# Optimization experiments

Hardware: AMD Instinct MI355X
Metric: run time of the kernel (lower is better)

## Reference

```python
import jax, jax.numpy as jnp
import numpy as np

V, D, T, H, L, B = 50257, 1024, 1024, 16, 6, 2
HS = D // H  # 64
EPS = 1e-5


def setup_inputs() -> dict:
    key = jax.random.key(0)
    ks = jax.random.split(key, 16)
    s = 0.02
    n = lambda k, sh: jax.random.normal(k, sh, jnp.float32) * s
    return {
        'idx': jax.random.randint(ks[0], (B, T), 0, V),
        'targets': jax.random.randint(ks[1], (B, T), 0, V),
        'tok_emb': n(ks[2], (V, D)),
        'pos_emb': n(ks[3], (T, D)),
        'wq': n(ks[4], (L, H, D, HS)),
        'wk': n(ks[5], (L, H, D, HS)),
        'wv': n(ks[6], (L, H, D, HS)),
        'wproj': n(ks[7], (L, D, D)),
        'bproj': jnp.zeros((L, D), jnp.float32),
        'ln1_g': jnp.ones((L, D), jnp.float32),
        'ln1_b': jnp.zeros((L, D), jnp.float32),
        'ln2_g': jnp.ones((L, D), jnp.float32),
        'ln2_b': jnp.zeros((L, D), jnp.float32),
        'w1': n(ks[8], (L, D, 4 * D)),
        'b1': jnp.zeros((L, 4 * D), jnp.float32),
        'w2': n(ks[9], (L, 4 * D, D)),
        'b2': jnp.zeros((L, D), jnp.float32),
        'lnf_g': jnp.ones((D,), jnp.float32),
        'lnf_b': jnp.zeros((D,), jnp.float32),
        'lm_w': n(ks[10], (D, V)),
        'lm_b': jnp.zeros((V,), jnp.float32),
    }


def _layernorm(x, g, b):
    mu = jnp.mean(x, axis=-1, keepdims=True)
    var = jnp.var(x, axis=-1, keepdims=True)
    return (x - mu) * jax.lax.rsqrt(var + EPS) * g + b


def _forward(idx, targets, tok_emb, pos_emb, wq, wk, wv, wproj, bproj,
             ln1_g, ln1_b, ln2_g, ln2_b, w1, b1, w2, b2, lnf_g, lnf_b, lm_w, lm_b):
    t = idx.shape[1]
    x = tok_emb[idx] + pos_emb[:t]  # [B,T,D]
    causal = jnp.tril(jnp.ones((t, t), bool))  # [T,T]
    neg_inf = jnp.float32(-jnp.inf)

    def block(x, p):
        (wq_l, wk_l, wv_l, wp_l, bp_l, g1, b1_ln, g2, b2_ln, wf1, bf1, wf2, bf2) = p
        h = _layernorm(x, g1, b1_ln)
        q = jnp.einsum('btd,hdk->bhtk', h, wq_l)
        k = jnp.einsum('btd,hdk->bhtk', h, wk_l)
        v = jnp.einsum('btd,hdk->bhtk', h, wv_l)
        scores = jnp.einsum('bhtk,bhsk->bhts', q, k) * (HS ** -0.5)
        scores = jnp.where(causal, scores, neg_inf)
        attn = jax.nn.softmax(scores, axis=-1)  # dropout p=0.0
        o = jnp.einsum('bhts,bhsk->bhtk', attn, v)
        o = o.transpose(0, 2, 1, 3).reshape(x.shape[0], t, H * HS)  # concat heads
        x = x + o @ wp_l + bp_l
        h2 = _layernorm(x, g2, b2_ln)
        x = x + jax.nn.relu(h2 @ wf1 + bf1) @ wf2 + bf2
        return x, None

    x, _ = jax.lax.scan(block, x, (wq, wk, wv, wproj, bproj,
                                   ln1_g, ln1_b, ln2_g, ln2_b, w1, b1, w2, b2))
    x = _layernorm(x, lnf_g, lnf_b)
    logits = x @ lm_w + lm_b  # [B,T,V]
    logp = jax.nn.log_softmax(logits, axis=-1)
    loss = -jnp.mean(jnp.take_along_axis(logp, targets[..., None], axis=-1))
    return logits, loss


def reference(idx, targets, tok_emb, pos_emb, wq, wk, wv, wproj, bproj,
              ln1_g, ln1_b, ln2_g, ln2_b, w1, b1, w2, b2, lnf_g, lnf_b, lm_w, lm_b):
    return _forward(idx, targets, tok_emb, pos_emb, wq, wk, wv, wproj, bproj,
                    ln1_g, ln1_b, ln2_g, ln2_b, w1, b1, w2, b2, lnf_g, lnf_b, lm_w, lm_b)
```

## Files before the change

kernel.cpp:

```cpp
#include <hip/hip_runtime.h>
#include <cstdint>
#include <cstddef>

typedef unsigned short u16;
typedef unsigned int u32;
typedef __bf16 bf16x8 __attribute__((ext_vector_type(8)));
typedef float f32x4 __attribute__((ext_vector_type(4)));
typedef short short8_t __attribute__((ext_vector_type(8)));

#define NV 50257
#define NVPAD 50304
#define NBLK_LM 393
#define ND 1024
#define NT 1024
#define NH 16
#define NL 6
#define NB 2
#define NM 2048
#define NF 4096
#define EPSLN 1e-5f

__device__ __forceinline__ u16 f2bf(float f) {
    unsigned u = __float_as_uint(f);
    return (u16)((u + 0x7fffu + ((u >> 16) & 1u)) >> 16);
}
__device__ __forceinline__ float bf2f(u16 h) {
    return __uint_as_float(((unsigned)h) << 16);
}
__device__ __forceinline__ u32 pack2bf(float lo, float hi) {
    return (u32)f2bf(lo) | ((u32)f2bf(hi) << 16);
}

__device__ __forceinline__ void gload_lds16(const u16* g, u16* l) {
    __builtin_amdgcn_global_load_lds((const __attribute__((address_space(1))) void*)g,
                                     (__attribute__((address_space(3))) void*)l, 16, 0, 0);
}

__device__ __forceinline__ float wave_reduce_sum(float v) {
#pragma unroll
    for (int off = 32; off >= 1; off >>= 1) v += __shfl_xor(v, off, 64);
    return v;
}

__global__ __launch_bounds__(256) void k_embed(const int* __restrict__ idx,
                                               const float* __restrict__ tok,
                                               const float* __restrict__ pos,
                                               float* __restrict__ x) {
    int m = blockIdx.x;
    int t = m & (NT - 1);
    int tokid = idx[m];
    int d = threadIdx.x * 4;
    float4 a = *(const float4*)(tok + (size_t)tokid * ND + d);
    float4 p = *(const float4*)(pos + (size_t)t * ND + d);
    a.x += p.x; a.y += p.y; a.z += p.z; a.w += p.w;
    *(float4*)(x + (size_t)m * ND + d) = a;
}

__global__ __launch_bounds__(256) void k_layernorm(const float* __restrict__ x,
                                                   const float* __restrict__ g,
                                                   const float* __restrict__ b,
                                                   u16* __restrict__ outb) {
    int m = blockIdx.x;
    int d = threadIdx.x * 4;
    const float4 v = *(const float4*)(x + (size_t)m * ND + d);
    float s = v.x + v.y + v.z + v.w;
    float q = v.x * v.x + v.y * v.y + v.z * v.z + v.w * v.w;
    s = wave_reduce_sum(s);
    q = wave_reduce_sum(q);
    __shared__ float ss[4], sq[4];
    int lane = threadIdx.x & 63, w = threadIdx.x >> 6;
    if (lane == 0) { ss[w] = s; sq[w] = q; }
    __syncthreads();
    s = ss[0] + ss[1] + ss[2] + ss[3];
    q = sq[0] + sq[1] + sq[2] + sq[3];
    float mu = s * (1.0f / ND);
    float var = q * (1.0f / ND) - mu * mu;
    float rstd = rsqrtf(var + EPSLN);
    float4 gg = *(const float4*)(g + d);
    float4 bb = *(const float4*)(b + d);
    ushort4 pk;
    pk.x = f2bf((v.x - mu) * rstd * gg.x + bb.x);
    pk.y = f2bf((v.y - mu) * rstd * gg.y + bb.y);
    pk.z = f2bf((v.z - mu) * rstd * gg.z + bb.z);
    pk.w = f2bf((v.w - mu) * rstd * gg.w + bb.w);
    *(ushort4*)(outb + (size_t)m * ND + d) = pk;
}

__global__ __launch_bounds__(256) void k_wtrans(const float* __restrict__ W,
                                                u16* __restrict__ Wt,
                                                int K, int N, int Npad, int hs, int ld) {
    __shared__ float t[32][33];
    const int nb = blockIdx.x << 5, kb = blockIdx.y << 5;
    const int tx = threadIdx.x & 31, tq = threadIdx.x >> 5;
    const int n = nb + tx;
    if (n < N) {
        const int head = n / hs, nc = n - head * hs;
        const float* src = W + (size_t)head * K * hs + nc;
#pragma unroll
        for (int i = 0; i < 4; ++i)
            t[(tq << 2) + i][tx] = src[(size_t)(kb + (tq << 2) + i) * ld];
    } else {
#pragma unroll
        for (int i = 0; i < 4; ++i) t[(tq << 2) + i][tx] = 0.f;
    }
    __syncthreads();
#pragma unroll
    for (int i = 0; i < 4; ++i) {
        const int nn = nb + (tq << 2) + i;
        if (nn < Npad) Wt[(size_t)nn * K + kb + tx] = f2bf(t[tx][(tq << 2) + i]);
    }
}

__global__ __launch_bounds__(256) void k_wtrans_qkv(const float* __restrict__ Wq,
                                                    const float* __restrict__ Wk,
                                                    const float* __restrict__ Wv,
                                                    u16* __restrict__ Wt) {
    __shared__ float t[32][33];
    const float* W = (blockIdx.z == 0) ? Wq : (blockIdx.z == 1) ? Wk : Wv;
    u16* dst = Wt + (size_t)blockIdx.z * ND * ND;
    const int nb = blockIdx.x << 5, kb = blockIdx.y << 5;
    const int tx = threadIdx.x & 31, tq = threadIdx.x >> 5;
    const int n = nb + tx;
    {
        const int head = n >> 6, nc = n & 63;
        const float* src = W + (size_t)head * ND * 64 + nc;
#pragma unroll
        for (int i = 0; i < 4; ++i)
            t[(tq << 2) + i][tx] = src[(size_t)(kb + (tq << 2) + i) * 64];
    }
    __syncthreads();
#pragma unroll
    for (int i = 0; i < 4; ++i) {
        const int nn = nb + (tq << 2) + i;
        dst[(size_t)nn * ND + kb + tx] = f2bf(t[tx][(tq << 2) + i]);
    }
}

__global__ __launch_bounds__(256) void k_vtrans(const u16* __restrict__ qkv,
                                                u16* __restrict__ vt) {
    __shared__ u16 L[64][72];
    const int tt = blockIdx.x, bh = blockIdx.y;
    const int b = bh >> 4, h = bh & 15;
    const int tid = threadIdx.x;
    const int tr = tid >> 2, dc = (tid & 3) << 4;
    const u16* src = qkv + (size_t)(b * NT + tt * 64 + tr) * 3072 + 2048 + h * 64 + dc;
    short8_t v0 = *(const short8_t*)src;
    short8_t v1 = *(const short8_t*)(src + 8);
#pragma unroll
    for (int j = 0; j < 8; ++j) { L[tr][dc + j] = (u16)v0[j]; L[tr][dc + 8 + j] = (u16)v1[j]; }
    __syncthreads();
    const int dr = tid >> 2, tc = (tid & 3) << 4;
    union { u16 us[16]; short8_t v[2]; } tmp;
#pragma unroll
    for (int j = 0; j < 16; ++j) tmp.us[j] = L[tc + j][dr];
    u16* dst = vt + ((size_t)bh * 64 + dr) * NT + tt * 64 + tc;
    *(short8_t*)dst = tmp.v[0];
    *(short8_t*)(dst + 8) = tmp.v[1];
}

__global__ __launch_bounds__(512) void k_gemm_lm(
    const u16* __restrict__ A, const u16* __restrict__ Bt,
    const float* __restrict__ bias,
    float* __restrict__ Cf,
    float* __restrict__ pmax_g, float* __restrict__ psum_g,
    int K, int N, int ldc)
{
    __shared__ u16 As[2][256 * 32];
    __shared__ u16 Bs[2][128 * 32];
    const int lin = blockIdx.y * 8 + blockIdx.x;
    const int nwg = (int)gridDim.y * 8;
    const int cpx = nwg >> 3;
    const int swz = (lin & 7) * cpx + (lin >> 3);
    const int m0 = (swz & 7) * 256;
    const int n0 = (swz >> 3) * 128;
    const int tid = threadIdx.x;
    const int lane = tid & 63, w = tid >> 6;
    const int wr = w >> 1, wc = w & 1;
    const int lr = lane & 15, kg = lane >> 4;

    const int srow = lane >> 2;
    const int scol = (((lane & 3) ^ ((lane >> 3) & 3)) << 3);
    const u16* gA0 = A + (size_t)(m0 + w * 16 + srow) * K + scol;
    const u16* gA1 = gA0 + (size_t)128 * K;
    const u16* gB0 = Bt + (size_t)(n0 + w * 16 + srow) * K + scol;

    f32x4 acc[4][4] = {};
    const int nt = K >> 5;

    gload_lds16(gA0, &As[0][w * 512]);
    gload_lds16(gA1, &As[0][4096 + w * 512]);
    gload_lds16(gB0, &Bs[0][w * 512]);
    __syncthreads();

    int cur = 0;
    for (int t = 0; t < nt; ++t) {
        if (t + 1 < nt) {
            const int ko = (t + 1) << 5;
            gload_lds16(gA0 + ko, &As[cur ^ 1][w * 512]);
            gload_lds16(gA1 + ko, &As[cur ^ 1][4096 + w * 512]);
            gload_lds16(gB0 + ko, &Bs[cur ^ 1][w * 512]);
        }
        bf16x8 af[4], bfr[4];
        const int rsw = ((kg ^ ((lr >> 1) & 3)) << 3);
#pragma unroll
        for (int mi = 0; mi < 4; ++mi)
            af[mi] = *(const bf16x8*)&As[cur][(wr * 64 + mi * 16 + lr) * 32 + rsw];
#pragma unroll
        for (int ni = 0; ni < 4; ++ni)
            bfr[ni] = *(const bf16x8*)&Bs[cur][(wc * 64 + ni * 16 + lr) * 32 + rsw];
#pragma unroll
        for (int mi = 0; mi < 4; ++mi)
#pragma unroll
            for (int ni = 0; ni < 4; ++ni)
                acc[mi][ni] = __builtin_amdgcn_mfma_f32_16x16x32_bf16(af[mi], bfr[ni], acc[mi][ni], 0, 0, 0);
        __syncthreads();
        cur ^= 1;
    }

#pragma unroll
    for (int mi = 0; mi < 4; ++mi)
#pragma unroll
        for (int ni = 0; ni < 4; ++ni)
#pragma unroll
            for (int r = 0; r < 4; ++r) {
                const int row = m0 + wr * 64 + mi * 16 + kg * 4 + r;
                const int col = n0 + wc * 64 + ni * 16 + lr;
                if (col >= N) continue;
                acc[mi][ni][r] += bias[col];
                Cf[(size_t)row * ldc + col] = acc[mi][ni][r];
            }

    float* redm = (float*)As;
    float* reds = redm + 512;
#pragma unroll
    for (int mi = 0; mi < 4; ++mi)
#pragma unroll
        for (int r = 0; r < 4; ++r) {
            float vmax = -3.0e38f;
#pragma unroll
            for (int ni = 0; ni < 4; ++ni) {
                const int col = n0 + wc * 64 + ni * 16 + lr;
                vmax = fmaxf(vmax, (col < N) ? acc[mi][ni][r] : -3.0e38f);
            }
            vmax = fmaxf(vmax, __shfl_xor(vmax, 1));
            vmax = fmaxf(vmax, __shfl_xor(vmax, 2));
            vmax = fmaxf(vmax, __shfl_xor(vmax, 4));
            vmax = fmaxf(vmax, __shfl_xor(vmax, 8));
            if (lr == 0) redm[wc * 256 + wr * 64 + mi * 16 + kg * 4 + r] = vmax;
        }
    __syncthreads();
#pragma unroll
    for (int mi = 0; mi < 4; ++mi)
#pragma unroll
        for (int r = 0; r < 4; ++r) {
            const int rloc = wr * 64 + mi * 16 + kg * 4 + r;
            const float M = fmaxf(redm[rloc], redm[256 + rloc]);
            float s = 0.f;
#pragma unroll
            for (int ni = 0; ni < 4; ++ni) {
                const int col = n0 + wc * 64 + ni * 16 + lr;
                if (col < N) s += __expf(acc[mi][ni][r] - M);
            }
            s += __shfl_xor(s, 1);
            s += __shfl_xor(s, 2);
            s += __shfl_xor(s, 4);
            s += __shfl_xor(s, 8);
            if (lr == 0) reds[wc * 256 + rloc] = s;
        }
    __syncthreads();
    if (tid < 256) {
        const float M = fmaxf(redm[tid], redm[256 + tid]);
        const float S = reds[tid] + reds[256 + tid];
        const int nblk = n0 >> 7;
        pmax_g[(size_t)nblk * NM + m0 + tid] = M;
        psum_g[(size_t)nblk * NM + m0 + tid] = S;
    }
}

template <bool RELU, bool NBOUND, bool OUTBF16>
__global__ __launch_bounds__(256) void k_mfma_gemm(
    const u16* __restrict__ A, const u16* __restrict__ Bt,
    const float* __restrict__ bias,
    float* __restrict__ Cf, u16* __restrict__ Cb,
    int K, int N, int ldc)
{
    __shared__ u16 As[2][128 * 32];
    __shared__ u16 Bs[2][128 * 32];
    const int lin = blockIdx.y * 16 + blockIdx.x;
    const int nwg = (int)gridDim.y * 16;
    const int cpx = nwg >> 3;
    const int swz = (lin & 7) * cpx + (lin >> 3);
    const int m0 = (swz & 15) * 128;
    const int n0 = (swz >> 4) * 128;
    const int tid = threadIdx.x;
    const int lane = tid & 63, wv = tid >> 6;
    const int wr = wv >> 1, wc = wv & 1;
    const int lr = lane & 15, kg = lane >> 4;

    const int srow = lane >> 2;
    const int scol = (((lane & 3) ^ ((lane >> 3) & 3)) << 3);
    const u16* gA0 = A + (size_t)(m0 + wv * 16 + srow) * K + scol;
    const u16* gA1 = gA0 + (size_t)64 * K;
    const u16* gB0 = Bt + (size_t)(n0 + wv * 16 + srow) * K + scol;
    const u16* gB1 = gB0 + (size_t)64 * K;

    f32x4 acc[4][4] = {};
    const int nt = K >> 5;

    gload_lds16(gA0, &As[0][wv * 512]);
    gload_lds16(gA1, &As[0][2048 + wv * 512]);
    gload_lds16(gB0, &Bs[0][wv * 512]);
    gload_lds16(gB1, &Bs[0][2048 + wv * 512]);
    __syncthreads();

    int cur = 0;
    for (int t = 0; t < nt; ++t) {
        if (t + 1 < nt) {
            const int ko = (t + 1) << 5;
            gload_lds16(gA0 + ko, &As[cur ^ 1][wv * 512]);
            gload_lds16(gA1 + ko, &As[cur ^ 1][2048 + wv * 512]);
            gload_lds16(gB0 + ko, &Bs[cur ^ 1][wv * 512]);
            gload_lds16(gB1 + ko, &Bs[cur ^ 1][2048 + wv * 512]);
        }
        bf16x8 af[4], bfr[4];
        const int rsw = ((kg ^ ((lr >> 1) & 3)) << 3);
#pragma unroll
        for (int mi = 0; mi < 4; ++mi) {
            const int R = wr * 64 + mi * 16 + lr;
            af[mi] = *(const bf16x8*)&As[cur][R * 32 + rsw];
        }
#pragma unroll
        for (int ni = 0; ni < 4; ++ni) {
            const int R = wc * 64 + ni * 16 + lr;
            bfr[ni] = *(const bf16x8*)&Bs[cur][R * 32 + rsw];
        }
#pragma unroll
        for (int mi = 0; mi < 4; ++mi)
#pragma unroll
            for (int ni = 0; ni < 4; ++ni)
                acc[mi][ni] = __builtin_amdgcn_mfma_f32_16x16x32_bf16(af[mi], bfr[ni], acc[mi][ni], 0, 0, 0);
        __syncthreads();
        cur ^= 1;
    }
#pragma unroll
    for (int mi = 0; mi < 4; ++mi) {
#pragma unroll
        for (int ni = 0; ni < 4; ++ni) {
#pragma unroll
            for (int r = 0; r < 4; ++r) {
                const int row = m0 + wr * 64 + mi * 16 + kg * 4 + r;
                const int col = n0 + wc * 64 + ni * 16 + lr;
                if (NBOUND && col >= N) continue;
                float c = acc[mi][ni][r];
                if (bias) c += bias[col];
                if (RELU) c = fmaxf(c, 0.f);
                if (OUTBF16) Cb[(size_t)row * ldc + col] = f2bf(c);
                else         Cf[(size_t)row * ldc + col] = c;
            }
        }
    }
}

__global__ __launch_bounds__(256) void k_gemm_ksplit(
    const u16* __restrict__ A, const u16* __restrict__ Bt,
    float* __restrict__ P,
    int Khalf, int Ktot, int ldc)
{
    __shared__ u16 As[2][128 * 32];
    __shared__ u16 Bs[2][128 * 32];
    const int z = blockIdx.z;
    const int lin = blockIdx.y * 16 + blockIdx.x;
    const int nwg = (int)gridDim.y * 16;
    const int cpx = nwg >> 3;
    const int swz = (lin & 7) * cpx + (lin >> 3);
    const int m0 = (swz & 15) * 128;
    const int n0 = (swz >> 4) * 128;
    const int tid = threadIdx.x;
    const int lane = tid & 63, wv = tid >> 6;
    const int wr = wv >> 1, wc = wv & 1;
    const int lr = lane & 15, kg = lane >> 4;

    const int srow = lane >> 2;
    const int scol = (((lane & 3) ^ ((lane >> 3) & 3)) << 3);
    const int koff = z * Khalf;
    const u16* gA0 = A + (size_t)(m0 + wv * 16 + srow) * Ktot + koff + scol;
    const u16* gA1 = gA0 + (size_t)64 * Ktot;
    const u16* gB0 = Bt + (size_t)(n0 + wv * 16 + srow) * Ktot + koff + scol;
    const u16* gB1 = gB0 + (size_t)64 * Ktot;
    float* Pz = P + (size_t)z * NM * ldc;

    f32x4 acc[4][4] = {};
    const int nt = Khalf >> 5;

    gload_lds16(gA0, &As[0][wv * 512]);
    gload_lds16(gA1, &As[0][2048 + wv * 512]);
    gload_lds16(gB0, &Bs[0][wv * 512]);
    gload_lds16(gB1, &Bs[0][2048 + wv * 512]);
    __syncthreads();

    int cur = 0;
    for (int t = 0; t < nt; ++t) {
        if (t + 1 < nt) {
            const int ko = (t + 1) << 5;
            gload_lds16(gA0 + ko, &As[cur ^ 1][wv * 512]);
            gload_lds16(gA1 + ko, &As[cur ^ 1][2048 + wv * 512]);
            gload_lds16(gB0 + ko, &Bs[cur ^ 1][wv * 512]);
            gload_lds16(gB1 + ko, &Bs[cur ^ 1][2048 + wv * 512]);
        }
        bf16x8 af[4], bfr[4];
        const int rsw = ((kg ^ ((lr >> 1) & 3)) << 3);
#pragma unroll
        for (int mi = 0; mi < 4; ++mi) {
            const int R = wr * 64 + mi * 16 + lr;
            af[mi] = *(const bf16x8*)&As[cur][R * 32 + rsw];
        }
#pragma unroll
        for (int ni = 0; ni < 4; ++ni) {
            const int R = wc * 64 + ni * 16 + lr;
            bfr[ni] = *(const bf16x8*)&Bs[cur][R * 32 + rsw];
        }
#pragma unroll
        for (int mi = 0; mi < 4; ++mi)
#pragma unroll
            for (int ni = 0; ni < 4; ++ni)
                acc[mi][ni] = __builtin_amdgcn_mfma_f32_16x16x32_bf16(af[mi], bfr[ni], acc[mi][ni], 0, 0, 0);
        __syncthreads();
        cur ^= 1;
    }
#pragma unroll
    for (int mi = 0; mi < 4; ++mi)
#pragma unroll
        for (int ni = 0; ni < 4; ++ni)
#pragma unroll
            for (int r = 0; r < 4; ++r) {
                const int row = m0 + wr * 64 + mi * 16 + kg * 4 + r;
                const int col = n0 + wc * 64 + ni * 16 + lr;
                Pz[(size_t)row * ldc + col] = acc[mi][ni][r];
            }
}

__global__ __launch_bounds__(256) void k_combine(const float* __restrict__ p,
                                                 const float* __restrict__ bias,
                                                 float* __restrict__ x) {
    const int m = blockIdx.x;
    const int d = threadIdx.x * 4;
    float4 a  = *(const float4*)(x + (size_t)m * ND + d);
    float4 q0 = *(const float4*)(p + (size_t)m * ND + d);
    float4 q1 = *(const float4*)(p + (size_t)NM * ND + (size_t)m * ND + d);
    float4 bb = *(const float4*)(bias + d);
    a.x += q0.x + q1.x + bb.x;
    a.y += q0.y + q1.y + bb.y;
    a.z += q0.z + q1.z + bb.z;
    a.w += q0.w + q1.w + bb.w;
    *(float4*)(x + (size_t)m * ND + d) = a;
}

template <bool RELU, bool RESID, bool OUTBF16>
__global__ __launch_bounds__(256) void k_gemm_n64(
    const u16* __restrict__ A, const u16* __restrict__ Bt,
    const float* __restrict__ bias, const float* __restrict__ resid,
    float* __restrict__ Cf, u16* __restrict__ Cb,
    int K, int ldc)
{
    __shared__ u16 As[2][128 * 32];
    __shared__ u16 Bs[2][64 * 32];
    const int lin = blockIdx.y * 16 + blockIdx.x;
    const int nwg = (int)gridDim.y * 16;
    const int cpx = nwg >> 3;
    const int swz = (lin & 7) * cpx + (lin >> 3);
    const int m0 = (swz & 15) * 128;
    const int n0 = (swz >> 4) * 64;
    const int tid = threadIdx.x;
    const int lane = tid & 63, wv = tid >> 6;
    const int lr = lane & 15, kg = lane >> 4;

    const int srow = lane >> 2;
    const int scol = (((lane & 3) ^ ((lane >> 3) & 3)) << 3);
    const u16* gA0 = A + (size_t)(m0 + wv * 32 + srow) * K + scol;
    const u16* gA1 = gA0 + (size_t)16 * K;
    const u16* gB0 = Bt + (size_t)(n0 + wv * 16 + srow) * K + scol;

    f32x4 acc[2][4] = {};
    const int nt = K >> 5;

    gload_lds16(gA0, &As[0][wv * 1024]);
    gload_lds16(gA1, &As[0][wv * 1024 + 512]);
    gload_lds16(gB0, &Bs[0][wv * 512]);
    __syncthreads();

    int cur = 0;
    for (int t = 0; t < nt; ++t) {
        if (t + 1 < nt) {
            const int ko = (t + 1) << 5;
            gload_lds16(gA0 + ko, &As[cur ^ 1][wv * 1024]);
            gload_lds16(gA1 + ko, &As[cur ^ 1][wv * 1024 + 512]);
            gload_lds16(gB0 + ko, &Bs[cur ^ 1][wv * 512]);
        }
        bf16x8 af[2], bfr[4];
        const int rsw = ((kg ^ ((lr >> 1) & 3)) << 3);
#pragma unroll
        for (int mi = 0; mi < 2; ++mi)
            af[mi] = *(const bf16x8*)&As[cur][(wv * 32 + mi * 16 + lr) * 32 + rsw];
#pragma unroll
        for (int ni = 0; ni < 4; ++ni)
            bfr[ni] = *(const bf16x8*)&Bs[cur][(ni * 16 + lr) * 32 + rsw];
#pragma unroll
        for (int mi = 0; mi < 2; ++mi)
#pragma unroll
            for (int ni = 0; ni < 4; ++ni)
                acc[mi][ni] = __builtin_amdgcn_mfma_f32_16x16x32_bf16(af[mi], bfr[ni], acc[mi][ni], 0, 0, 0);
        __syncthreads();
        cur ^= 1;
    }
#pragma unroll
    for (int mi = 0; mi < 2; ++mi) {
#pragma unroll
        for (int ni = 0; ni < 4; ++ni) {
#pragma unroll
            for (int r = 0; r < 4; ++r) {
                const int row = m0 + wv * 32 + mi * 16 + kg * 4 + r;
                const int col = n0 + ni * 16 + lr;
                float c = acc[mi][ni][r];
                if (bias) c += bias[col];
                if (RELU) c = fmaxf(c, 0.f);
                if (RESID) c += resid[(size_t)row * ldc + col];
                if (OUTBF16) Cb[(size_t)row * ldc + col] = f2bf(c);
                else         Cf[(size_t)row * ldc + col] = c;
            }
        }
    }
}

__global__ __launch_bounds__(256) void k_attn_mfma(const u16* __restrict__ qkv,
                                                   const u16* __restrict__ vt,
                                                   u16* __restrict__ ob) {
    const int qt = (blockIdx.y < 16) ? (int)blockIdx.x : 15 - (int)blockIdx.x;
    const int bh = blockIdx.y;
    const int b = bh >> 4, h = bh & 15;
    const int tid = threadIdx.x;
    const int lane = tid & 63, w = tid >> 6;
    const int lr = lane & 15, kg = lane >> 4;

    __shared__ u16 Qs[64 * 64];
    __shared__ u16 Ks[2][64 * 64];
    __shared__ u16 Vs[2][64 * 64];

    const int srow8 = lane >> 3;
    const int csw = ((lane & 7) ^ srow8) << 3;

    {
        const int r0 = w * 8 + srow8;
        gload_lds16(qkv + (size_t)(b * NT + qt * 64 + r0) * 3072 + h * 64 + csw, &Qs[w * 512]);
        gload_lds16(qkv + (size_t)(b * NT + qt * 64 + 32 + r0) * 3072 + h * 64 + csw, &Qs[2048 + w * 512]);
    }
#define STAGE_KV(bb, st)                                                                            \
    {                                                                                               \
        const int r0_ = w * 8 + srow8;                                                              \
        gload_lds16(qkv + (size_t)(b * NT + (st) * 64 + r0_) * 3072 + 1024 + h * 64 + csw,          \
                    &Ks[bb][w * 512]);                                                              \
        gload_lds16(qkv + (size_t)(b * NT + (st) * 64 + 32 + r0_) * 3072 + 1024 + h * 64 + csw,     \
                    &Ks[bb][2048 + w * 512]);                                                       \
        gload_lds16(vt + ((size_t)bh * 64 + r0_) * NT + (st) * 64 + csw, &Vs[bb][w * 512]);         \
        gload_lds16(vt + ((size_t)bh * 64 + 32 + r0_) * NT + (st) * 64 + csw,                       \
                    &Vs[bb][2048 + w * 512]);                                                       \
    }
    STAGE_KV(0, 0);
    __syncthreads();

    bf16x8 qf[2];
    {
        const int qrow = w * 16 + lr;
#pragma unroll
        for (int ds_ = 0; ds_ < 2; ++ds_)
            qf[ds_] = *(const bf16x8*)&Qs[qrow * 64 + ((((ds_ << 2) + kg) ^ (lr & 7)) << 3)];
    }

    float mstate = -3.0e38f, lstate = 0.f;
    f32x4 acc_o[4] = {};
    const int qg = qt * 64 + w * 16 + lr;

    int cur = 0;
    for (int st = 0; st <= qt; ++st) {
        if (st < qt) STAGE_KV(cur ^ 1, st + 1);
        const bool diag = (st == qt);
        const int milim = diag ? w : 3;

        f32x4 acc_s[4] = {};
#pragma unroll
        for (int mi = 0; mi < 4; ++mi) {
            if (mi <= milim) {
                const int srw = mi * 16 + lr;
#pragma unroll
                for (int ds_ = 0; ds_ < 2; ++ds_) {
                    bf16x8 kf = *(const bf16x8*)&Ks[cur][srw * 64 + ((((ds_ << 2) + kg) ^ (lr & 7)) << 3)];
                    acc_s[mi] = __builtin_amdgcn_mfma_f32_16x16x32_bf16(kf, qf[ds_], acc_s[mi], 0, 0, 0);
                }
            }
        }
        float tilemax = -3.0e38f;
#pragma unroll
        for (int mi = 0; mi < 4; ++mi)
#pragma unroll
            for (int r = 0; r < 4; ++r) {
                float x_ = acc_s[mi][r] * 0.125f;
                const int sg = st * 64 + mi * 16 + kg * 4 + r;
                if (mi > milim || sg > qg) x_ = -3.0e38f;
                acc_s[mi][r] = x_;
                tilemax = fmaxf(tilemax, x_);
            }
        tilemax = fmaxf(tilemax, __shfl_xor(tilemax, 16));
        tilemax = fmaxf(tilemax, __shfl_xor(tilemax, 32));
        const float mnew = fmaxf(mstate, tilemax);
        const float rfac = __expf(mstate - mnew);
        mstate = mnew;

        float psum = 0.f;
        u32 pk[4][2];
#pragma unroll
        for (int mi = 0; mi < 4; ++mi) {
            float p0 = __expf(acc_s[mi][0] - mnew);
            float p1 = __expf(acc_s[mi][1] - mnew);
            float p2 = __expf(acc_s[mi][2] - mnew);
            float p3 = __expf(acc_s[mi][3] - mnew);
            psum += p0 + p1 + p2 + p3;
            pk[mi][0] = pack2bf(p0, p1);
            pk[mi][1] = pack2bf(p2, p3);
        }
        psum += __shfl_xor(psum, 16);
        psum += __shfl_xor(psum, 32);
        lstate = lstate * rfac + psum;

        float rf[4];
#pragma unroll
        for (int r = 0; r < 4; ++r) rf[r] = __shfl(rfac, kg * 4 + r);
#pragma unroll
        for (int ni = 0; ni < 4; ++ni)
#pragma unroll
            for (int r = 0; r < 4; ++r) acc_o[ni][r] *= rf[r];

        const int src0 = ((kg & 1) << 5) + lr;
        const int src1 = src0 + 16;
#pragma unroll
        for (int ks_ = 0; ks_ < 2; ++ks_) {
            const u32 lo_a = __shfl((int)pk[ks_ * 2][0], src0);
            const u32 lo_b = __shfl((int)pk[ks_ * 2][1], src0);
            const u32 lo_c = __shfl((int)pk[ks_ * 2][0], src1);
            const u32 lo_d = __shfl((int)pk[ks_ * 2][1], src1);
            const u32 hi_a = __shfl((int)pk[ks_ * 2 + 1][0], src0);
            const u32 hi_b = __shfl((int)pk[ks_ * 2 + 1][1], src0);
            const u32 hi_c = __shfl((int)pk[ks_ * 2 + 1][0], src1);
            const u32 hi_d = __shfl((int)pk[ks_ * 2 + 1][1], src1);
            union { u32 u[4]; bf16x8 v; } pa;
            pa.u[0] = (kg & 2) ? hi_a : lo_a;
            pa.u[1] = (kg & 2) ? hi_b : lo_b;
            pa.u[2] = (kg & 2) ? hi_c : lo_c;
            pa.u[3] = (kg & 2) ? hi_d : lo_d;
#pragma unroll
            for (int ni = 0; ni < 4; ++ni) {
                const int drow = ni * 16 + lr;
                bf16x8 vf = *(const bf16x8*)&Vs[cur][drow * 64 + ((((ks_ << 2) + kg) ^ (lr & 7)) << 3)];
                acc_o[ni] = __builtin_amdgcn_mfma_f32_16x16x32_bf16(pa.v, vf, acc_o[ni], 0, 0, 0);
            }
        }
        __syncthreads();
        cur ^= 1;
    }

    float il[4];
#pragma unroll
    for (int r = 0; r < 4; ++r) il[r] = 1.0f / __shfl(lstate, kg * 4 + r);
#pragma unroll
    for (int ni = 0; ni < 4; ++ni)
#pragma unroll
        for (int r = 0; r < 4; ++r) {
            const int q2 = qt * 64 + w * 16 + kg * 4 + r;
            ob[(size_t)(b * NT + q2) * ND + h * 64 + ni * 16 + lr] = f2bf(acc_o[ni][r] * il[r]);
        }
#undef STAGE_KV
}

__global__ __launch_bounds__(256) void k_losscombine(const float* __restrict__ pmax,
                                                     const float* __restrict__ psum,
                                                     const float* __restrict__ logits,
                                                     const int* __restrict__ targets,
                                                     float* __restrict__ rl) {
    const int row = blockIdx.x * 4 + (threadIdx.x >> 6);
    const int lane = threadIdx.x & 63;
    float M = -3.0e38f;
    for (int j = lane; j < NBLK_LM; j += 64) M = fmaxf(M, pmax[(size_t)j * NM + row]);
#pragma unroll
    for (int off = 32; off >= 1; off >>= 1) M = fmaxf(M, __shfl_xor(M, off, 64));
    float S = 0.f;
    for (int j = lane; j < NBLK_LM; j += 64)
        S += psum[(size_t)j * NM + row] * __expf(pmax[(size_t)j * NM + row] - M);
    S = wave_reduce_sum(S);
    if (lane == 0)
        rl[row] = M + logf(S) - logits[(size_t)row * NV + targets[row]];
}

__global__ __launch_bounds__(256) void k_lossreduce(const float* __restrict__ rl,
                                                    float* __restrict__ out_loss) {
    int tid = threadIdx.x;
    float s = 0.f;
    for (int j = tid; j < NM; j += 256) s += rl[j];
    s = wave_reduce_sum(s);
    __shared__ float sv[4];
    int lane = tid & 63, w = tid >> 6;
    if (lane == 0) sv[w] = s;
    __syncthreads();
    if (tid == 0) out_loss[0] = (sv[0] + sv[1] + sv[2] + sv[3]) * (1.0f / NM);
}

extern "C" void kernel_launch(void* const* d_in, const int* in_sizes, int n_in,
                              void* d_out, int out_size, void* d_ws, size_t ws_size,
                              hipStream_t stream) {
    const int* idx      = (const int*)d_in[0];
    const int* targets  = (const int*)d_in[1];
    const float* tok    = (const float*)d_in[2];
    const float* pos    = (const float*)d_in[3];
    const float* wq     = (const float*)d_in[4];
    const float* wk     = (const float*)d_in[5];
    const float* wv     = (const float*)d_in[6];
    const float* wproj  = (const float*)d_in[7];
    const float* bproj  = (const float*)d_in[8];
    const float* ln1_g  = (const float*)d_in[9];
    const float* ln1_b  = (const float*)d_in[10];
    const float* ln2_g  = (const float*)d_in[11];
    const float* ln2_b  = (const float*)d_in[12];
    const float* w1     = (const float*)d_in[13];
    const float* b1     = (const float*)d_in[14];
    const float* w2     = (const float*)d_in[15];
    const float* b2     = (const float*)d_in[16];
    const float* lnf_g  = (const float*)d_in[17];
    const float* lnf_b  = (const float*)d_in[18];
    const float* lm_w   = (const float*)d_in[19];
    const float* lm_b   = (const float*)d_in[20];
    float* out = (float*)d_out;

    char* wsb = (char*)d_ws;
    auto alloc = [&](size_t bytes) { char* p = wsb; wsb += (bytes + 255) & ~(size_t)255; return p; };
    float* x     = (float*)alloc((size_t)NM * ND * 4);
    u16* h_bf    = (u16*)  alloc((size_t)NM * ND * 2);
    float* rl    = (float*)alloc((size_t)NM * 4);
    float* pmax  = (float*)alloc((size_t)NBLK_LM * NM * 4);
    float* psum  = (float*)alloc((size_t)NBLK_LM * NM * 4);
    char* region = (char*)alloc((size_t)NVPAD * ND * 2);
    u16* qkv_bf = (u16*)(region);
    u16* vt_bf  = (u16*)(region + ((size_t)12 << 20));
    u16* ob_bf  = (u16*)(region + ((size_t)16 << 20));
    u16* hid_bf = (u16*)(region + ((size_t)20 << 20));
    u16* wqkv_t = (u16*)(region + ((size_t)36 << 20));
    u16* wp_t   = (u16*)(region + ((size_t)42 << 20));
    u16* w1_t   = (u16*)(region + ((size_t)44 << 20));
    u16* w2_t   = (u16*)(region + ((size_t)52 << 20));
    float* p01  = (float*)(region + ((size_t)60 << 20));
    u16* lm_t   = (u16*)(region);

    k_embed<<<NM, 256, 0, stream>>>(idx, tok, pos, x);

    for (int l = 0; l < NL; ++l) {
        const float* wq_l = wq + (size_t)l * NH * ND * 64;
        const float* wk_l = wk + (size_t)l * NH * ND * 64;
        const float* wv_l = wv + (size_t)l * NH * ND * 64;
        const float* wp_l = wproj + (size_t)l * ND * ND;
        const float* bp_l = bproj + (size_t)l * ND;
        const float* w1_l = w1 + (size_t)l * ND * NF;
        const float* b1_l = b1 + (size_t)l * NF;
        const float* w2_l = w2 + (size_t)l * NF * ND;
        const float* b2_l = b2 + (size_t)l * ND;

        k_layernorm<<<NM, 256, 0, stream>>>(x, ln1_g + (size_t)l * ND, ln1_b + (size_t)l * ND, h_bf);

        k_wtrans_qkv<<<dim3(32, 32, 3), 256, 0, stream>>>(wq_l, wk_l, wv_l, wqkv_t);
        k_mfma_gemm<false, false, true><<<dim3(16, 24), 256, 0, stream>>>(
            h_bf, wqkv_t, nullptr, nullptr, qkv_bf, ND, 3 * ND, 3 * ND);

        k_vtrans<<<dim3(NT / 64, NB * NH), 256, 0, stream>>>(qkv_bf, vt_bf);
        k_attn_mfma<<<dim3(NT / 64, NB * NH), 256, 0, stream>>>(qkv_bf, vt_bf, ob_bf);

        k_wtrans<<<dim3(ND / 32, ND / 32), 256, 0, stream>>>(wp_l, wp_t, ND, ND, ND, ND, ND);
        k_gemm_n64<false, true, false><<<dim3(16, 16), 256, 0, stream>>>(
            ob_bf, wp_t, bp_l, x, x, nullptr, ND, ND);

        k_layernorm<<<NM, 256, 0, stream>>>(x, ln2_g + (size_t)l * ND, ln2_b + (size_t)l * ND, h_bf);

        k_wtrans<<<dim3(NF / 32, ND / 32), 256, 0, stream>>>(w1_l, w1_t, ND, NF, NF, NF, NF);
        k_mfma_gemm<true, false, true><<<dim3(16, 32), 256, 0, stream>>>(
            h_bf, w1_t, b1_l, nullptr, hid_bf, ND, NF, NF);

        k_wtrans<<<dim3(ND / 32, NF / 32), 256, 0, stream>>>(w2_l, w2_t, NF, ND, ND, ND, ND);
        k_gemm_ksplit<<<dim3(16, 8, 2), 256, 0, stream>>>(
            hid_bf, w2_t, p01, NF / 2, NF, ND);
        k_combine<<<NM, 256, 0, stream>>>(p01, b2_l, x);
    }

    k_layernorm<<<NM, 256, 0, stream>>>(x, lnf_g, lnf_b, h_bf);

    k_wtrans<<<dim3(NVPAD / 32, ND / 32), 256, 0, stream>>>(lm_w, lm_t, ND, NV, NVPAD, NV, NV);
    k_gemm_lm<<<dim3(8, NVPAD / 128), 512, 0, stream>>>(
        h_bf, lm_t, lm_b, out, pmax, psum, ND, NV, NV);

    k_losscombine<<<NM / 4, 256, 0, stream>>>(pmax, psum, out, targets, rl);
    k_lossreduce<<<1, 256, 0, stream>>>(rl, out + (size_t)NM * NV);
}
```

Before: 1.663 ms.

## Generalize LM-head GEMM to 256x128 tiles for FFN, merge weight transposes

Turns the 512-thread 256x128-tile LM-head GEMM into a template with optional ReLU, bf16 output, K-split and softmax-partial epilogues. It then runs the FFN up-projection with it, and the down-projection as a 4-way K-split with a four-input combine kernel. The three per-layer weight transposes (proj, w1, w2) are merged into one launch, cutting launch count. Bigger tiles give more data reuse per block but fewer blocks (256 for the FFN1 GEMM), and the 4-way split adds extra fp32 partial traffic.

After: 1.613 ms. -3.0%, faster.

```diff
diff --git a/kernel.cpp b/kernel.cpp
--- a/kernel.cpp
+++ b/kernel.cpp
@@ -136,6 +136,31 @@
     }
 }
 
+__global__ __launch_bounds__(256) void k_wtrans3(const float* __restrict__ Wp,
+                                                 const float* __restrict__ W1,
+                                                 const float* __restrict__ W2,
+                                                 u16* __restrict__ Wpt,
+                                                 u16* __restrict__ W1t,
+                                                 u16* __restrict__ W2t) {
+    __shared__ float t[32][33];
+    int bid = blockIdx.x;
+    const float* W; u16* Wt; int K, N, nb, kb;
+    if (bid < 1024)      { W = Wp; Wt = Wpt; K = ND; N = ND; bid -= 0;
+                           nb = (bid & 31) << 5; kb = (bid >> 5) << 5; }
+    else if (bid < 5120) { W = W1; Wt = W1t; K = ND; N = NF; bid -= 1024;
+                           nb = (bid & 127) << 5; kb = (bid >> 7) << 5; }
+    else                 { W = W2; Wt = W2t; K = NF; N = ND; bid -= 5120;
+                           nb = (bid & 31) << 5; kb = (bid >> 5) << 5; }
+    const int tx = threadIdx.x & 31, tq = threadIdx.x >> 5;
+#pragma unroll
+    for (int i = 0; i < 4; ++i)
+        t[(tq << 2) + i][tx] = W[(size_t)(kb + (tq << 2) + i) * N + nb + tx];
+    __syncthreads();
+#pragma unroll
+    for (int i = 0; i < 4; ++i)
+        Wt[(size_t)(nb + (tq << 2) + i) * K + kb + tx] = f2bf(t[tx][(tq << 2) + i]);
+}
+
 __global__ __launch_bounds__(256) void k_vtrans(const u16* __restrict__ qkv,
                                                 u16* __restrict__ vt) {
     __shared__ u16 L[64][72];
@@ -158,17 +183,18 @@
     *(short8_t*)(dst + 8) = tmp.v[1];
 }
 
-__global__ __launch_bounds__(512) void k_gemm_lm(
+template <bool RELU, bool NBOUND, bool PART, bool KSPLIT, bool OUTBF16>
+__global__ __launch_bounds__(512) void k_gemm_big(
     const u16* __restrict__ A, const u16* __restrict__ Bt,
     const float* __restrict__ bias,
-    float* __restrict__ Cf,
+    float* __restrict__ Cf, u16* __restrict__ Cb,
     float* __restrict__ pmax_g, float* __restrict__ psum_g,
-    int K, int N, int ldc)
+    int Ksub, int Ktot, int N, int ldc)
 {
     __shared__ u16 As[2][256 * 32];
     __shared__ u16 Bs[2][128 * 32];
-    const int lin = blockIdx.y * 8 + blockIdx.x;
-    const int nwg = (int)gridDim.y * 8;
+    const int lin = blockIdx.y * (int)gridDim.x + blockIdx.x;
+    const int nwg = (int)gridDim.x * (int)gridDim.y;
     const int cpx = nwg >> 3;
     const int swz = (lin & 7) * cpx + (lin >> 3);
     const int m0 = (swz & 7) * 256;
@@ -180,12 +206,13 @@
 
     const int srow = lane >> 2;
     const int scol = (((lane & 3) ^ ((lane >> 3) & 3)) << 3);
-    const u16* gA0 = A + (size_t)(m0 + w * 16 + srow) * K + scol;
-    const u16* gA1 = gA0 + (size_t)128 * K;
-    const u16* gB0 = Bt + (size_t)(n0 + w * 16 + srow) * K + scol;
+    const int koff = KSPLIT ? (int)blockIdx.z * Ksub : 0;
+    const u16* gA0 = A + (size_t)(m0 + w * 16 + srow) * Ktot + koff + scol;
+    const u16* gA1 = gA0 + (size_t)128 * Ktot;
+    const u16* gB0 = Bt + (size_t)(n0 + w * 16 + srow) * Ktot + koff + scol;
 
     f32x4 acc[4][4] = {};
-    const int nt = K >> 5;
+    const int nt = Ksub >> 5;
 
     gload_lds16(gA0, &As[0][w * 512]);
     gload_lds16(gA1, &As[0][4096 + w * 512]);
@@ -217,6 +244,7 @@
         cur ^= 1;
     }
 
+    float* Cz = KSPLIT ? (Cf + (size_t)blockIdx.z * NM * ldc) : Cf;
 #pragma unroll
     for (int mi = 0; mi < 4; ++mi)
 #pragma unroll
@@ -225,55 +253,61 @@
             for (int r = 0; r < 4; ++r) {
                 const int row = m0 + wr * 64 + mi * 16 + kg * 4 + r;
                 const int col = n0 + wc * 64 + ni * 16 + lr;
-                if (col >= N) continue;
-                acc[mi][ni][r] += bias[col];
-                Cf[(size_t)row * ldc + col] = acc[mi][ni][r];
+                if (NBOUND && col >= N) continue;
+                float c = acc[mi][ni][r];
+                if (bias) c += bias[col];
+                if (RELU) c = fmaxf(c, 0.f);
+                if (PART) acc[mi][ni][r] = c;
+                if (OUTBF16) Cb[(size_t)row * ldc + col] = f2bf(c);
+                else         Cz[(size_t)row * ldc + col] = c;
             }
 
-    float* redm = (float*)As;
-    float* reds = redm + 512;
-#pragma unroll
-    for (int mi = 0; mi < 4; ++mi)
-#pragma unroll
-        for (int r = 0; r < 4; ++r) {
-            float vmax = -3.0e38f;
-#pragma unroll
-            for (int ni = 0; ni < 4; ++ni) {
-                const int col = n0 + wc * 64 + ni * 16 + lr;
-                vmax = fmaxf(vmax, (col < N) ? acc[mi][ni][r] : -3.0e38f);
+    if constexpr (PART) {
+        float* redm = (float*)As;
+        float* reds = redm + 512;
+#pragma unroll
+        for (int mi = 0; mi < 4; ++mi)
+#pragma unroll
+            for (int r = 0; r < 4; ++r) {
+                float vmax = -3.0e38f;
+#pragma unroll
+                for (int ni = 0; ni < 4; ++ni) {
+                    const int col = n0 + wc * 64 + ni * 16 + lr;
+                    vmax = fmaxf(vmax, (col < N) ? acc[mi][ni][r] : -3.0e38f);
+                }
+                vmax = fmaxf(vmax, __shfl_xor(vmax, 1));
+                vmax = fmaxf(vmax, __shfl_xor(vmax, 2));
+                vmax = fmaxf(vmax, __shfl_xor(vmax, 4));
+                vmax = fmaxf(vmax, __shfl_xor(vmax, 8));
+                if (lr == 0) redm[wc * 256 + wr * 64 + mi * 16 + kg * 4 + r] = vmax;
             }
-            vmax = fmaxf(vmax, __shfl_xor(vmax, 1));
-            vmax = fmaxf(vmax, __shfl_xor(vmax, 2));
-            vmax = fmaxf(vmax, __shfl_xor(vmax, 4));
-            vmax = fmaxf(vmax, __shfl_xor(vmax, 8));
-            if (lr == 0) redm[wc * 256 + wr * 64 + mi * 16 + kg * 4 + r] = vmax;
-        }
-    __syncthreads();
-#pragma unroll
-    for (int mi = 0; mi < 4; ++mi)
-#pragma unroll
-        for (int r = 0; r < 4; ++r) {
-            const int rloc = wr * 64 + mi * 16 + kg * 4 + r;
-            const float M = fmaxf(redm[rloc], redm[256 + rloc]);
-            float s = 0.f;
-#pragma unroll
-            for (int ni = 0; ni < 4; ++ni) {
-                const int col = n0 + wc * 64 + ni * 16 + lr;
-                if (col < N) s += __expf(acc[mi][ni][r] - M);
+        __syncthreads();
+#pragma unroll
+        for (int mi = 0; mi < 4; ++mi)
+#pragma unroll
+            for (int r = 0; r < 4; ++r) {
+                const int rloc = wr * 64 + mi * 16 + kg * 4 + r;
+                const float M = fmaxf(redm[rloc], redm[256 + rloc]);
+                float s = 0.f;
+#pragma unroll
+                for (int ni = 0; ni < 4; ++ni) {
+                    const int col = n0 + wc * 64 + ni * 16 + lr;
+                    if (col < N) s += __expf(acc[mi][ni][r] - M);
+                }
+                s += __shfl_xor(s, 1);
+                s += __shfl_xor(s, 2);
+                s += __shfl_xor(s, 4);
+                s += __shfl_xor(s, 8);
+                if (lr == 0) reds[wc * 256 + rloc] = s;
             }
-            s += __shfl_xor(s, 1);
-            s += __shfl_xor(s, 2);
-            s += __shfl_xor(s, 4);
-            s += __shfl_xor(s, 8);
-            if (lr == 0) reds[wc * 256 + rloc] = s;
-        }
-    __syncthreads();
-    if (tid < 256) {
-        const float M = fmaxf(redm[tid], redm[256 + tid]);
-        const float S = reds[tid] + reds[256 + tid];
-        const int nblk = n0 >> 7;
-        pmax_g[(size_t)nblk * NM + m0 + tid] = M;
-        psum_g[(size_t)nblk * NM + m0 + tid] = S;
+        __syncthreads();
+        if (tid < 256) {
+            const float M = fmaxf(redm[tid], redm[256 + tid]);
+            const float S = reds[tid] + reds[256 + tid];
+            const int nblk = n0 >> 7;
+            pmax_g[(size_t)nblk * NM + m0 + tid] = M;
+            psum_g[(size_t)nblk * NM + m0 + tid] = S;
+        }
     }
 }
 
@@ -361,98 +395,23 @@
     }
 }
 
-__global__ __launch_bounds__(256) void k_gemm_ksplit(
-    const u16* __restrict__ A, const u16* __restrict__ Bt,
-    float* __restrict__ P,
-    int Khalf, int Ktot, int ldc)
-{
-    __shared__ u16 As[2][128 * 32];
-    __shared__ u16 Bs[2][128 * 32];
-    const int z = blockIdx.z;
-    const int lin = blockIdx.y * 16 + blockIdx.x;
-    const int nwg = (int)gridDim.y * 16;
-    const int cpx = nwg >> 3;
-    const int swz = (lin & 7) * cpx + (lin >> 3);
-    const int m0 = (swz & 15) * 128;
-    const int n0 = (swz >> 4) * 128;
-    const int tid = threadIdx.x;
-    const int lane = tid & 63, wv = tid >> 6;
-    const int wr = wv >> 1, wc = wv & 1;
-    const int lr = lane & 15, kg = lane >> 4;
-
-    const int srow = lane >> 2;
-    const int scol = (((lane & 3) ^ ((lane >> 3) & 3)) << 3);
-    const int koff = z * Khalf;
-    const u16* gA0 = A + (size_t)(m0 + wv * 16 + srow) * Ktot + koff + scol;
-    const u16* gA1 = gA0 + (size_t)64 * Ktot;
-    const u16* gB0 = Bt + (size_t)(n0 + wv * 16 + srow) * Ktot + koff + scol;
-    const u16* gB1 = gB0 + (size_t)64 * Ktot;
-    float* Pz = P + (size_t)z * NM * ldc;
-
-    f32x4 acc[4][4] = {};
-    const int nt = Khalf >> 5;
-
-    gload_lds16(gA0, &As[0][wv * 512]);
-    gload_lds16(gA1, &As[0][2048 + wv * 512]);
-    gload_lds16(gB0, &Bs[0][wv * 512]);
-    gload_lds16(gB1, &Bs[0][2048 + wv * 512]);
-    __syncthreads();
-
-    int cur = 0;
-    for (int t = 0; t < nt; ++t) {
-        if (t + 1 < nt) {
-            const int ko = (t + 1) << 5;
-            gload_lds16(gA0 + ko, &As[cur ^ 1][wv * 512]);
-            gload_lds16(gA1 + ko, &As[cur ^ 1][2048 + wv * 512]);
-            gload_lds16(gB0 + ko, &Bs[cur ^ 1][wv * 512]);
-            gload_lds16(gB1 + ko, &Bs[cur ^ 1][2048 + wv * 512]);
-        }
-        bf16x8 af[4], bfr[4];
-        const int rsw = ((kg ^ ((lr >> 1) & 3)) << 3);
-#pragma unroll
-        for (int mi = 0; mi < 4; ++mi) {
-            const int R = wr * 64 + mi * 16 + lr;
-            af[mi] = *(const bf16x8*)&As[cur][R * 32 + rsw];
-        }
-#pragma unroll
-        for (int ni = 0; ni < 4; ++ni) {
-            const int R = wc * 64 + ni * 16 + lr;
-            bfr[ni] = *(const bf16x8*)&Bs[cur][R * 32 + rsw];
-        }
-#pragma unroll
-        for (int mi = 0; mi < 4; ++mi)
-#pragma unroll
-            for (int ni = 0; ni < 4; ++ni)
-                acc[mi][ni] = __builtin_amdgcn_mfma_f32_16x16x32_bf16(af[mi], bfr[ni], acc[mi][ni], 0, 0, 0);
-        __syncthreads();
-        cur ^= 1;
-    }
-#pragma unroll
-    for (int mi = 0; mi < 4; ++mi)
-#pragma unroll
-        for (int ni = 0; ni < 4; ++ni)
-#pragma unroll
-            for (int r = 0; r < 4; ++r) {
-                const int row = m0 + wr * 64 + mi * 16 + kg * 4 + r;
-                const int col = n0 + wc * 64 + ni * 16 + lr;
-                Pz[(size_t)row * ldc + col] = acc[mi][ni][r];
-            }
-}
-
-__global__ __launch_bounds__(256) void k_combine(const float* __restrict__ p,
-                                                 const float* __restrict__ bias,
-                                                 float* __restrict__ x) {
+__global__ __launch_bounds__(256) void k_combine4(const float* __restrict__ p,
+                                                  const float* __restrict__ bias,
+                                                  float* __restrict__ x) {
     const int m = blockIdx.x;
     const int d = threadIdx.x * 4;
-    float4 a  = *(const float4*)(x + (size_t)m * ND + d);
-    float4 q0 = *(const float4*)(p + (size_t)m * ND + d);
-    float4 q1 = *(const float4*)(p + (size_t)NM * ND + (size_t)m * ND + d);
+    const size_t off = (size_t)m * ND + d;
+    float4 a  = *(const float4*)(x + off);
+    float4 q0 = *(const float4*)(p + off);
+    float4 q1 = *(const float4*)(p + (size_t)NM * ND + off);
+    float4 q2 = *(const float4*)(p + (size_t)2 * NM * ND + off);
+    float4 q3 = *(const float4*)(p + (size_t)3 * NM * ND + off);
     float4 bb = *(const float4*)(bias + d);
-    a.x += q0.x + q1.x + bb.x;
-    a.y += q0.y + q1.y + bb.y;
-    a.z += q0.z + q1.z + bb.z;
-    a.w += q0.w + q1.w + bb.w;
-    *(float4*)(x + (size_t)m * ND + d) = a;
+    a.x += ((q0.x + q1.x) + (q2.x + q3.x)) + bb.x;
+    a.y += ((q0.y + q1.y) + (q2.y + q3.y)) + bb.y;
+    a.z += ((q0.z + q1.z) + (q2.z + q3.z)) + bb.z;
+    a.w += ((q0.w + q1.w) + (q2.w + q3.w)) + bb.w;
+    *(float4*)(x + off) = a;
 }
 
 template <bool RELU, bool RESID, bool OUTBF16>
@@ -753,7 +712,7 @@
     u16* wp_t   = (u16*)(region + ((size_t)42 << 20));
     u16* w1_t   = (u16*)(region + ((size_t)44 << 20));
     u16* w2_t   = (u16*)(region + ((size_t)52 << 20));
-    float* p01  = (float*)(region + ((size_t)60 << 20));
+    float* p03  = (float*)(region + ((size_t)60 << 20));
     u16* lm_t   = (u16*)(region);
 
     k_embed<<<NM, 256, 0, stream>>>(idx, tok, pos, x);
@@ -772,33 +731,32 @@
         k_layernorm<<<NM, 256, 0, stream>>>(x, ln1_g + (size_t)l * ND, ln1_b + (size_t)l * ND, h_bf);
 
         k_wtrans_qkv<<<dim3(32, 32, 3), 256, 0, stream>>>(wq_l, wk_l, wv_l, wqkv_t);
+        k_wtrans3<<<9216, 256, 0, stream>>>(wp_l, w1_l, w2_l, wp_t, w1_t, w2_t);
+
         k_mfma_gemm<false, false, true><<<dim3(16, 24), 256, 0, stream>>>(
             h_bf, wqkv_t, nullptr, nullptr, qkv_bf, ND, 3 * ND, 3 * ND);
 
         k_vtrans<<<dim3(NT / 64, NB * NH), 256, 0, stream>>>(qkv_bf, vt_bf);
         k_attn_mfma<<<dim3(NT / 64, NB * NH), 256, 0, stream>>>(qkv_bf, vt_bf, ob_bf);
 
-        k_wtrans<<<dim3(ND / 32, ND / 32), 256, 0, stream>>>(wp_l, wp_t, ND, ND, ND, ND, ND);
         k_gemm_n64<false, true, false><<<dim3(16, 16), 256, 0, stream>>>(
             ob_bf, wp_t, bp_l, x, x, nullptr, ND, ND);
 
         k_layernorm<<<NM, 256, 0, stream>>>(x, ln2_g + (size_t)l * ND, ln2_b + (size_t)l * ND, h_bf);
 
-        k_wtrans<<<dim3(NF / 32, ND / 32), 256, 0, stream>>>(w1_l, w1_t, ND, NF, NF, NF, NF);
-        k_mfma_gemm<true, false, true><<<dim3(16, 32), 256, 0, stream>>>(
-            h_bf, w1_t, b1_l, nullptr, hid_bf, ND, NF, NF);
-
-        k_wtrans<<<dim3(ND / 32, NF / 32), 256, 0, stream>>>(w2_l, w2_t, NF, ND, ND, ND, ND);
-        k_gemm_ksplit<<<dim3(16, 8, 2), 256, 0, stream>>>(
-            hid_bf, w2_t, p01, NF / 2, NF, ND);
-        k_combine<<<NM, 256, 0, stream>>>(p01, b2_l, x);
+        k_gemm_big<true, false, false, false, true><<<dim3(8, 32), 512, 0, stream>>>(
+            h_bf, w1_t, b1_l, nullptr, hid_bf, nullptr, nullptr, ND, ND, NF, NF);
+
+        k_gemm_big<false, false, false, true, false><<<dim3(8, 8, 4), 512, 0, stream>>>(
+            hid_bf, w2_t, nullptr, p03, nullptr, nullptr, nullptr, NF / 4, NF, ND, ND);
+        k_combine4<<<NM, 256, 0, stream>>>(p03, b2_l, x);
     }
 
     k_layernorm<<<NM, 256, 0, stream>>>(x, lnf_g, lnf_b, h_bf);
 
     k_wtrans<<<dim3(NVPAD / 32, ND / 32), 256, 0, stream>>>(lm_w, lm_t, ND, NV, NVPAD, NV, NV);
-    k_gemm_lm<<<dim3(8, NVPAD / 128), 512, 0, stream>>>(
-        h_bf, lm_t, lm_b, out, pmax, psum, ND, NV, NV);
+    k_gemm_big<false, true, true, false, false><<<dim3(8, NVPAD / 128), 512, 0, stream>>>(
+        h_bf, lm_t, lm_b, out, nullptr, pmax, psum, ND, ND, NV, NV);
 
     k_losscombine<<<NM / 4, 256, 0, stream>>>(pmax, psum, out, targets, rl);
     k_lossreduce<<<1, 256, 0, stream>>>(rl, out + (size_t)NM * NV);
```
